# Performance work log

Measured on AMD Instinct MI355X. Metric: run time of the kernel, lower is better.

## Reference

```python
import jax, jax.numpy as jnp
import numpy as np


def _conv1x1(x, w, b):
    # x: (B, C, H, W), w: (O, C), b: (O,) -> (B, O, H, W)
    return jnp.einsum('bchw,oc->bohw', x, w) + b[None, :, None, None]


def setup_inputs() -> dict:
    key = jax.random.key(0)
    ks = jax.random.split(key, 9)
    C, Cb = 256, 128
    B, H, W = 4, 64, 64
    s_in = 1.0 / np.sqrt(C)   # kaiming-uniform-ish scale for 1x1 convs
    s_bn = 1.0 / np.sqrt(Cb)
    return {
        'x': jax.random.normal(ks[0], (B, C, H, W), dtype=jnp.float32),
        'theta_w': jax.random.uniform(ks[1], (Cb, C), jnp.float32, -s_in, s_in),
        'theta_b': jax.random.uniform(ks[2], (Cb,), jnp.float32, -s_in, s_in),
        'phi_w': jax.random.uniform(ks[3], (Cb, C), jnp.float32, -s_in, s_in),
        'phi_b': jax.random.uniform(ks[4], (Cb,), jnp.float32, -s_in, s_in),
        'g_w': jax.random.uniform(ks[5], (Cb, C), jnp.float32, -s_in, s_in),
        'g_b': jax.random.uniform(ks[6], (Cb,), jnp.float32, -s_in, s_in),
        'W_w': jax.random.uniform(ks[7], (C, Cb), jnp.float32, -s_bn, s_bn),
        'W_b': jax.random.uniform(ks[8], (C,), jnp.float32, -s_bn, s_bn),
    }


def reference(x, theta_w, theta_b, phi_w, phi_b, g_w, g_b, W_w, W_b):
    B, C, H, Wd = x.shape
    Cb = theta_w.shape[0]
    # NOTE: the original uses raw torch.reshape (row-major), NOT transpose,
    # so (B, Cb, H, W) -> (B, H*W, Cb) scrambles channel/spatial layout.
    # We replicate that exactly with jnp.reshape.
    theta = _conv1x1(x, theta_w, theta_b).reshape(B, -1, Cb)   # (B, N, Cb)
    phi = _conv1x1(x, phi_w, phi_b).reshape(B, Cb, -1)         # (B, Cb, N)
    g = _conv1x1(x, g_w, g_b).reshape(B, -1, Cb)               # (B, N, Cb)
    scores = jnp.einsum('bnc,bcm->bnm', theta, phi)            # (B, N, N)
    attn = jax.nn.softmax(scores, axis=1)                      # softmax over dim=1 (unusual axis)
    y = jnp.einsum('bnm,bmc->bnc', attn, g)                    # (B, N, Cb)
    y = y.reshape(B, -1, H, Wd)                                # raw reshape back to (B, Cb, H, W)
    w = _conv1x1(y, W_w, W_b)                                  # (B, C, H, W)
    return w + x
```

## Files before the change

kernel.cpp:

```cpp
#include <hip/hip_runtime.h>
#include <math.h>

constexpr int CI = 256;
constexpr int CB = 128;
constexpr int HWD = 4096;
constexpr int NBATCH = 4;
constexpr int NN_ = 4096;
constexpr size_t U1 = (size_t)NBATCH * NN_ * CB;
constexpr size_t U_THETA = 0;
constexpr size_t U_PHIT  = U1;
constexpr size_t U_G     = 2 * U1;
constexpr size_t U_GT    = 3 * U1;
constexpr size_t U_Y     = 4 * U1;
constexpr size_t U_XT    = 4 * U1;
constexpr size_t U_WCAT  = 8 * U1;
constexpr size_t U_WW    = 8 * U1 + 98304;
constexpr size_t F_D     = (8 * U1 + 131072) / 2;

typedef short v8s __attribute__((ext_vector_type(8)));
typedef unsigned short u8s __attribute__((ext_vector_type(8)));
typedef float v4f __attribute__((ext_vector_type(4)));
typedef float v16f __attribute__((ext_vector_type(16)));
#define MFMA16(a, b, c) __builtin_amdgcn_mfma_f32_16x16x32_bf16(a, b, c, 0, 0, 0)
#define MFMA32(a, b, c) __builtin_amdgcn_mfma_f32_32x32x16_bf16(a, b, c, 0, 0, 0)

__device__ __forceinline__ unsigned short f2bf(float f) {
    union { float f; unsigned u; } v; v.f = f;
    unsigned r = v.u + 0x7fff + ((v.u >> 16) & 1);
    return (unsigned short)(r >> 16);
}
__device__ __forceinline__ float bf2f(unsigned short s) {
    union { unsigned u; float f; } v; v.u = (unsigned)s << 16;
    return v.f;
}

__global__ __launch_bounds__(256) void k0_xpose(
    const float* __restrict__ x, unsigned short* __restrict__ xT,
    const float* __restrict__ tw, const float* __restrict__ pw,
    const float* __restrict__ gw, const float* __restrict__ Ww,
    unsigned short* __restrict__ wcat, unsigned short* __restrict__ wwB)
{
    __shared__ unsigned short T[64 * 72];
    const int t = threadIdx.x;
    if (blockIdx.y == 4) {
        int wb = blockIdx.x + 64 * blockIdx.z;
        if (t < 128) {
            int e = (wb * 128 + t) * 4;
            const float* src; unsigned short* dst;
            if (e < 32768)       { src = tw + e;           dst = wcat + e; }
            else if (e < 65536)  { src = pw + (e - 32768); dst = wcat + e; }
            else if (e < 98304)  { src = gw + (e - 65536); dst = wcat + e; }
            else                 { src = Ww + (e - 98304); dst = wwB + (e - 98304); }
            float4 f = *(const float4*)src;
            ushort4 u;
            u.x = f2bf(f.x); u.y = f2bf(f.y); u.z = f2bf(f.z); u.w = f2bf(f.w);
            *(ushort4*)dst = u;
        }
        return;
    }
    const int hw0 = blockIdx.x * 64, c0 = blockIdx.y * 64, b = blockIdx.z;
    const float* xb = x + (size_t)b * CI * HWD;
    const int rr = t >> 4, cc = t & 15;
    #pragma unroll
    for (int pass = 0; pass < 4; pass++) {
        float4 f = *(const float4*)&xb[(size_t)(c0 + pass * 16 + rr) * HWD + hw0 + cc * 4];
        T[(cc * 4 + 0) * 72 + pass * 16 + rr] = f2bf(f.x);
        T[(cc * 4 + 1) * 72 + pass * 16 + rr] = f2bf(f.y);
        T[(cc * 4 + 2) * 72 + pass * 16 + rr] = f2bf(f.z);
        T[(cc * 4 + 3) * 72 + pass * 16 + rr] = f2bf(f.w);
    }
    __syncthreads();
    const int row = t >> 2, cs = (t & 3) * 16;
    unsigned short* dst = xT + (size_t)b * NN_ * CI;
    #pragma unroll
    for (int h = 0; h < 2; h++)
        *(u8s*)&dst[(size_t)(hw0 + row) * CI + c0 + cs + h * 8] =
            *(const u8s*)&T[row * 72 + cs + h * 8];
}

__global__ __launch_bounds__(256, 4) void k1_mfma(
    const unsigned short* __restrict__ xT, const unsigned short* __restrict__ wcat,
    const float* __restrict__ tb, const float* __restrict__ pb,
    const float* __restrict__ gb,
    unsigned short* __restrict__ thetaB, unsigned short* __restrict__ phiTB,
    unsigned short* __restrict__ gB)
{
    __shared__ unsigned short LdsX[64 * 268];
    unsigned short* T = LdsX;
    const int t = threadIdx.x;
    const int lane = t & 63, w = t >> 6;
    const int l31 = lane & 31, lh = lane >> 5;
    const int qj = w >> 1, qh = w & 1;
    const int hw0 = blockIdx.x * 64, j0 = blockIdx.y * 64, b = blockIdx.z;
    const int matId = j0 >> 7, jl0 = j0 & 127;
    const float* bvec = (matId == 0) ? tb : (matId == 1) ? pb : gb;
    const unsigned short* xb = xT + (size_t)b * NN_ * CI;

    {
        const int row = t >> 2, seg = t & 3;
        #pragma unroll
        for (int c8 = 0; c8 < 8; c8++)
            *(u8s*)&LdsX[row * 268 + seg * 64 + c8 * 8] =
                *(const u8s*)&xb[(size_t)(hw0 + row) * CI + seg * 64 + c8 * 8];
    }
    __syncthreads();

    v16f s = {};
    #pragma unroll
    for (int kt = 0; kt < 16; kt++) {
        v8s a = *(const v8s*)&wcat[(size_t)(j0 + qj * 32 + l31) * CI + kt * 16 + lh * 8];
        v8s bx = *(const v8s*)&LdsX[(qh * 32 + l31) * 268 + kt * 16 + lh * 8];
        s = MFMA32(a, bx, s);
    }

    if (matId != 1) {
        unsigned short* dst = ((matId == 0) ? thetaB : gB) + (size_t)b * CB * HWD;
        #pragma unroll
        for (int reg = 0; reg < 16; reg++) {
            int row = (reg & 3) + 8 * (reg >> 2) + 4 * lh;
            int cb = jl0 + qj * 32 + row;
            dst[(size_t)cb * HWD + hw0 + qh * 32 + l31] = f2bf(s[reg] + bvec[cb]);
        }
    } else {
        __syncthreads();
        #pragma unroll
        for (int reg = 0; reg < 16; reg++) {
            int row = (reg & 3) + 8 * (reg >> 2) + 4 * lh;
            T[(qh * 32 + l31) * 76 + qj * 32 + row] =
                f2bf(s[reg] + bvec[jl0 + qj * 32 + row]);
        }
        __syncthreads();
        unsigned short* dst = phiTB + (size_t)b * NN_ * CB;
        const int row = t >> 2, cs = (t & 3) * 16;
        #pragma unroll
        for (int h = 0; h < 2; h++)
            *(u8s*)&dst[(size_t)(hw0 + row) * CB + jl0 + cs + h * 8] =
                *(const u8s*)&T[row * 76 + cs + h * 8];
    }
}

__global__ __launch_bounds__(256, 2) void k2_colsum(
    const unsigned short* __restrict__ thetaB,
    const unsigned short* __restrict__ phiTB,
    float* __restrict__ Dout)
{
    __shared__ float part[4][128];
    const int t = threadIdx.x;
    const int lane = t & 63, w = t >> 6;
    const int ln = lane & 15, quad = lane >> 4;
    const int m0 = blockIdx.x * 128, q = blockIdx.y, b = blockIdx.z;
    const unsigned short* th = thetaB + (size_t)b * NN_ * CB;
    const unsigned short* ph = phiTB + (size_t)b * NN_ * CB;

    v8s bf[8][4];
    #pragma unroll
    for (int mt = 0; mt < 8; mt++)
        #pragma unroll
        for (int kt = 0; kt < 4; kt++)
            bf[mt][kt] = *(const v8s*)&ph[(size_t)(m0 + mt * 16 + ln) * CB + kt * 32 + quad * 8];

    float dsum[8] = {};
    const int nBeg = q * 1024 + w * 16, nEnd = q * 1024 + 1024;
    v8s af[4], afn[4];
    #pragma unroll
    for (int kt = 0; kt < 4; kt++)
        af[kt] = *(const v8s*)&th[(size_t)(nBeg + ln) * CB + kt * 32 + quad * 8];
    for (int n0 = nBeg; n0 < nEnd; n0 += 64) {
        int nn = (n0 + 64 < nEnd) ? n0 + 64 : nBeg;
        #pragma unroll
        for (int kt = 0; kt < 4; kt++)
            afn[kt] = *(const v8s*)&th[(size_t)(nn + ln) * CB + kt * 32 + quad * 8];
        #pragma unroll
        for (int mt = 0; mt < 8; mt++) {
            v4f s = {};
            #pragma unroll
            for (int kt = 0; kt < 4; kt++)
                s = MFMA16(af[kt], bf[mt][kt], s);
            #pragma unroll
            for (int r = 0; r < 4; r++)
                dsum[mt] += __expf(s[r]);
        }
        #pragma unroll
        for (int kt = 0; kt < 4; kt++) af[kt] = afn[kt];
    }
    #pragma unroll
    for (int mt = 0; mt < 8; mt++) {
        float v = dsum[mt];
        v += __shfl_xor(v, 16);
        v += __shfl_xor(v, 32);
        dsum[mt] = v;
    }
    if (quad == 0) {
        #pragma unroll
        for (int mt = 0; mt < 8; mt++) part[w][mt * 16 + ln] = dsum[mt];
    }
    __syncthreads();
    if (t < 128) {
        float v = part[0][t] + part[1][t] + part[2][t] + part[3][t];
        Dout[((size_t)q * NBATCH + b) * NN_ + m0 + t] = v;
    }
}

__global__ __launch_bounds__(256) void k1b_transpose_scale_g(
    const unsigned short* __restrict__ gB, const float* __restrict__ D,
    unsigned short* __restrict__ gTB)
{
    __shared__ unsigned short T[128 * 36];
    const int t = threadIdx.x;
    const int m0 = blockIdx.x * 32;
    const int b  = blockIdx.z;
    const unsigned short* F = gB + (size_t)b * CB * HWD;
    unsigned short* dst = gTB + (size_t)b * CB * HWD;
    const int mrow = t >> 3, cg = t & 7;
    {
        int m = m0 + mrow;
        float d = D[((size_t)0 * NBATCH + b) * NN_ + m]
                + D[((size_t)1 * NBATCH + b) * NN_ + m]
                + D[((size_t)2 * NBATCH + b) * NN_ + m]
                + D[((size_t)3 * NBATCH + b) * NN_ + m];
        float r = 1.0f / d;
        #pragma unroll
        for (int j8 = 0; j8 < 2; j8++) {
            int cbase = cg * 8 + j8 * 64;
            u8s u = *(const u8s*)&F[(size_t)m * CB + cbase];
            #pragma unroll
            for (int e = 0; e < 8; e++)
                T[(cbase + e) * 36 + mrow] = f2bf(bf2f(u[e]) * r);
        }
    }
    __syncthreads();
    const int c = t >> 1, mh = (t & 1) * 16;
    #pragma unroll
    for (int h8 = 0; h8 < 2; h8++)
        *(u8s*)&dst[(size_t)c * HWD + m0 + mh + h8 * 8] =
            *(const u8s*)&T[c * 36 + mh + h8 * 8];
}

__global__ __launch_bounds__(256, 3) void k3_attn(
    const unsigned short* __restrict__ thetaB,
    const unsigned short* __restrict__ phiTB,
    const unsigned short* __restrict__ gTB,
    unsigned short* __restrict__ Y)
{
    __shared__ unsigned short Lphi[2][64 * 132];
    __shared__ unsigned short Pl[2][64 * 68];
    const int t = threadIdx.x;
    const int lane = t & 63, w = t >> 6;
    const int l31 = lane & 31, lh = lane >> 5;
    const int qn = w & 1, qm = w >> 1;
    const int rowS = t >> 4, colS = t & 15;
    const int n0 = blockIdx.x * 64, q = blockIdx.y, b = blockIdx.z;
    const unsigned short* th = thetaB + (size_t)b * NN_ * CB;
    const unsigned short* ph = phiTB + (size_t)b * NN_ * CB;
    const unsigned short* gT = gTB + (size_t)b * CB * HWD;

    v8s ath[8];
    #pragma unroll
    for (int kt = 0; kt < 8; kt++)
        ath[kt] = *(const v8s*)&th[(size_t)(n0 + qn * 32 + l31) * CB + kt * 16 + lh * 8];

    const int mBeg = q * 1024;
    v8s preg[4];
    #pragma unroll
    for (int pass = 0; pass < 4; pass++)
        preg[pass] = *(const v8s*)&ph[(size_t)(mBeg + pass * 16 + rowS) * CB + colS * 8];
    #pragma unroll
    for (int pass = 0; pass < 4; pass++)
        *(v8s*)&Lphi[0][(pass * 16 + rowS) * 132 + colS * 8] = preg[pass];
    #pragma unroll
    for (int pass = 0; pass < 4; pass++)
        preg[pass] = *(const v8s*)&ph[(size_t)(mBeg + 64 + pass * 16 + rowS) * CB + colS * 8];
    __syncthreads();

    v16f yacc[2] = {};
    #pragma unroll 2
    for (int it = 0; it < 16; ++it) {
        const int cur = it & 1;
        const int m0 = mBeg + it * 64;
        v8s gfrag[4];
        #pragma unroll
        for (int ks = 0; ks < 4; ks++)
            gfrag[ks] = *(const v8s*)&gT[(size_t)(w * 32 + l31) * HWD + m0 + ks * 16 + lh * 8];
        v16f s = {};
        #pragma unroll
        for (int kt = 0; kt < 8; kt++) {
            v8s bphi = *(const v8s*)&Lphi[cur][(qm * 32 + l31) * 132 + kt * 16 + lh * 8];
            s = MFMA32(ath[kt], bphi, s);
        }
        #pragma unroll
        for (int pass = 0; pass < 4; pass++)
            *(v8s*)&Lphi[cur ^ 1][(pass * 16 + rowS) * 132 + colS * 8] = preg[pass];
        #pragma unroll
        for (int reg = 0; reg < 16; reg++) {
            int row = qn * 32 + (reg & 3) + 8 * (reg >> 2) + 4 * lh;
            Pl[cur][row * 68 + qm * 32 + l31] = f2bf(__expf(s[reg]));
        }
        __syncthreads();
        const int mP = mBeg + ((it + 2) & 15) * 64;
        #pragma unroll
        for (int pass = 0; pass < 4; pass++)
            preg[pass] = *(const v8s*)&ph[(size_t)(mP + pass * 16 + rowS) * CB + colS * 8];
        #pragma unroll
        for (int ks = 0; ks < 4; ks++)
            #pragma unroll
            for (int nt = 0; nt < 2; nt++) {
                v8s ap = *(const v8s*)&Pl[cur][(nt * 32 + l31) * 68 + ks * 16 + lh * 8];
                yacc[nt] = MFMA32(ap, gfrag[ks], yacc[nt]);
            }
    }
    unsigned short* yp = Y + ((size_t)q * NBATCH + b) * CB * HWD;
    #pragma unroll
    for (int nt = 0; nt < 2; nt++)
        #pragma unroll
        for (int reg = 0; reg < 16; reg++) {
            int row = (reg & 3) + 8 * (reg >> 2) + 4 * lh;
            yp[(size_t)(n0 + nt * 32 + row) * CB + w * 32 + l31] = f2bf(yacc[nt][reg]);
        }
}

__global__ __launch_bounds__(256, 2) void k4_mfma(
    const float* __restrict__ x, const unsigned short* __restrict__ wwB,
    const float* __restrict__ Wb, const unsigned short* __restrict__ Ybuf,
    float* __restrict__ out)
{
    __shared__ unsigned short Yt[64 * 136];
    const int t = threadIdx.x;
    const int lane = t & 63, w = t >> 6;
    const int ln = lane & 15, quad = lane >> 4;
    const int hw0 = blockIdx.x * 64, o0 = blockIdx.y * 128, b = blockIdx.z;

    const int cb = t >> 1, seg = (t & 1) * 32;
    #pragma unroll
    for (int g8 = 0; g8 < 4; g8++) {
        float sum[8] = {};
        #pragma unroll
        for (int q = 0; q < 4; q++) {
            u8s u = *(const u8s*)&Ybuf[((size_t)q * NBATCH + b) * CB * HWD +
                                       (size_t)cb * HWD + hw0 + seg + g8 * 8];
            #pragma unroll
            for (int j = 0; j < 8; j++) sum[j] += bf2f(u[j]);
        }
        #pragma unroll
        for (int j = 0; j < 8; j++)
            Yt[(seg + g8 * 8 + j) * 136 + cb] = f2bf(sum[j]);
    }
    __syncthreads();

    v8s aw[2][4];
    #pragma unroll
    for (int os = 0; os < 2; os++)
        #pragma unroll
        for (int kt = 0; kt < 4; kt++)
            aw[os][kt] = *(const v8s*)&wwB[(size_t)(o0 + w * 32 + os * 16 + ln) * CB + kt * 32 + quad * 8];

    v4f s[2][4] = {};
    #pragma unroll
    for (int kt = 0; kt < 4; kt++) {
        v8s by[4];
        #pragma unroll
        for (int mt = 0; mt < 4; mt++)
            by[mt] = *(const v8s*)&Yt[(mt * 16 + ln) * 136 + kt * 32 + quad * 8];
        #pragma unroll
        for (int os = 0; os < 2; os++)
            #pragma unroll
            for (int mt = 0; mt < 4; mt++)
                s[os][mt] = MFMA16(aw[os][kt], by[mt], s[os][mt]);
    }
    #pragma unroll
    for (int os = 0; os < 2; os++)
        #pragma unroll
        for (int mt = 0; mt < 4; mt++)
            #pragma unroll
            for (int r = 0; r < 4; r++) {
                int o = o0 + w * 32 + os * 16 + quad * 4 + r;
                size_t idx = (size_t)b * CI * HWD + (size_t)o * HWD + hw0 + mt * 16 + ln;
                out[idx] = s[os][mt][r] + Wb[o] + x[idx];
            }
}

extern "C" void kernel_launch(void* const* d_in, const int* in_sizes, int n_in,
                              void* d_out, int out_size, void* d_ws, size_t ws_size,
                              hipStream_t stream)
{
    const float* x  = (const float*)d_in[0];
    const float* tw = (const float*)d_in[1];
    const float* tb = (const float*)d_in[2];
    const float* pw = (const float*)d_in[3];
    const float* pb = (const float*)d_in[4];
    const float* gw = (const float*)d_in[5];
    const float* gb = (const float*)d_in[6];
    const float* Ww = (const float*)d_in[7];
    const float* Wb = (const float*)d_in[8];
    unsigned short* wsu = (unsigned short*)d_ws;
    float* wsf = (float*)d_ws;
    unsigned short* thetaB = wsu + U_THETA;
    unsigned short* phiTB  = wsu + U_PHIT;
    unsigned short* gB     = wsu + U_G;
    unsigned short* gTB    = wsu + U_GT;
    unsigned short* Ybuf   = wsu + U_Y;
    unsigned short* xTB    = wsu + U_XT;
    unsigned short* wcatB  = wsu + U_WCAT;
    unsigned short* wwB    = wsu + U_WW;
    float* Dbuf = wsf + F_D;
    float* out = (float*)d_out;
    dim3 blk(256, 1, 1);
    hipLaunchKernelGGL(k0_xpose, dim3(64, 5, NBATCH), blk, 0, stream,
                       x, xTB, tw, pw, gw, Ww, wcatB, wwB);
    hipLaunchKernelGGL(k1_mfma, dim3(64, 6, NBATCH), blk, 0, stream,
                       xTB, wcatB, tb, pb, gb, thetaB, phiTB, gB);
    hipLaunchKernelGGL(k2_colsum, dim3(32, 4, NBATCH), blk, 0, stream,
                       thetaB, phiTB, Dbuf);
    hipLaunchKernelGGL(k1b_transpose_scale_g, dim3(128, 1, NBATCH), blk, 0, stream,
                       gB, Dbuf, gTB);
    hipLaunchKernelGGL(k3_attn, dim3(64, 4, NBATCH), blk, 0, stream,
                       thetaB, phiTB, gTB, Ybuf);
    hipLaunchKernelGGL(k4_mfma, dim3(64, 2, NBATCH), blk, 0, stream,
                       x, wwB, Wb, Ybuf, out);
}
```

Measured before the change: 196.3 us.

## Keep attention probabilities in registers via permlane32 swap, widen n-tile to 128

```diff
diff --git a/kernel.cpp b/kernel.cpp
--- a/kernel.cpp
+++ b/kernel.cpp
@@ -19,6 +19,7 @@
 
 typedef short v8s __attribute__((ext_vector_type(8)));
 typedef unsigned short u8s __attribute__((ext_vector_type(8)));
+typedef unsigned int v4u __attribute__((ext_vector_type(4)));
 typedef float v4f __attribute__((ext_vector_type(4)));
 typedef float v16f __attribute__((ext_vector_type(16)));
 #define MFMA16(a, b, c) __builtin_amdgcn_mfma_f32_16x16x32_bf16(a, b, c, 0, 0, 0)
@@ -32,6 +33,22 @@
 __device__ __forceinline__ float bf2f(unsigned short s) {
     union { unsigned u; float f; } v; v.u = (unsigned)s << 16;
     return v.f;
+}
+__device__ __forceinline__ unsigned pack2bf(float lo, float hi) {
+    return (unsigned)f2bf(lo) | ((unsigned)f2bf(hi) << 16);
+}
+__device__ __forceinline__ void pl32swap(unsigned &a, unsigned &b) {
+    asm volatile("v_permlane32_swap_b32 %0, %1" : "+v"(a), "+v"(b));
+}
+__device__ __forceinline__ v8s pack_swap(float p0, float p1, float p2, float p3,
+                                         float p4, float p5, float p6, float p7) {
+    unsigned c0 = pack2bf(p0, p1), c1 = pack2bf(p2, p3);
+    unsigned c2 = pack2bf(p4, p5), c3 = pack2bf(p6, p7);
+    pl32swap(c0, c2);
+    pl32swap(c1, c3);
+    union { v4u u; v8s s; } r;
+    r.u[0] = c0; r.u[1] = c1; r.u[2] = c2; r.u[3] = c3;
+    return r.s;
 }
 
 __global__ __launch_bounds__(256) void k0_xpose(
@@ -236,20 +253,18 @@
             *(const u8s*)&T[c * 36 + mh + h8 * 8];
 }
 
-__global__ __launch_bounds__(256, 3) void k3_attn(
+__global__ __launch_bounds__(256, 2) void k3_attn(
     const unsigned short* __restrict__ thetaB,
     const unsigned short* __restrict__ phiTB,
     const unsigned short* __restrict__ gTB,
     unsigned short* __restrict__ Y)
 {
-    __shared__ unsigned short Lphi[2][64 * 132];
-    __shared__ unsigned short Pl[2][64 * 68];
+    __shared__ unsigned short Lphi[2][64 * 134];
     const int t = threadIdx.x;
     const int lane = t & 63, w = t >> 6;
     const int l31 = lane & 31, lh = lane >> 5;
-    const int qn = w & 1, qm = w >> 1;
     const int rowS = t >> 4, colS = t & 15;
-    const int n0 = blockIdx.x * 64, q = blockIdx.y, b = blockIdx.z;
+    const int n0 = blockIdx.x * 128, q = blockIdx.y, b = blockIdx.z;
     const unsigned short* th = thetaB + (size_t)b * NN_ * CB;
     const unsigned short* ph = phiTB + (size_t)b * NN_ * CB;
     const unsigned short* gT = gTB + (size_t)b * CB * HWD;
@@ -257,64 +272,80 @@
     v8s ath[8];
     #pragma unroll
     for (int kt = 0; kt < 8; kt++)
-        ath[kt] = *(const v8s*)&th[(size_t)(n0 + qn * 32 + l31) * CB + kt * 16 + lh * 8];
+        ath[kt] = *(const v8s*)&th[(size_t)(n0 + w * 32 + l31) * CB + kt * 16 + lh * 8];
 
     const int mBeg = q * 1024;
     v8s preg[4];
     #pragma unroll
-    for (int pass = 0; pass < 4; pass++)
-        preg[pass] = *(const v8s*)&ph[(size_t)(mBeg + pass * 16 + rowS) * CB + colS * 8];
-    #pragma unroll
-    for (int pass = 0; pass < 4; pass++)
-        *(v8s*)&Lphi[0][(pass * 16 + rowS) * 132 + colS * 8] = preg[pass];
-    #pragma unroll
-    for (int pass = 0; pass < 4; pass++)
-        preg[pass] = *(const v8s*)&ph[(size_t)(mBeg + 64 + pass * 16 + rowS) * CB + colS * 8];
-    __syncthreads();
-
-    v16f yacc[2] = {};
+    for (int p = 0; p < 4; p++)
+        preg[p] = *(const v8s*)&ph[(size_t)(mBeg + p * 16 + rowS) * CB + colS * 8];
+    #pragma unroll
+    for (int p = 0; p < 4; p++)
+        *(v8s*)&Lphi[0][(p * 16 + rowS) * 134 + colS * 8] = preg[p];
+    #pragma unroll
+    for (int p = 0; p < 4; p++)
+        preg[p] = *(const v8s*)&ph[(size_t)(mBeg + 64 + p * 16 + rowS) * CB + colS * 8];
+    __syncthreads();
+
+    v16f yacc[4] = {};
     #pragma unroll 2
     for (int it = 0; it < 16; ++it) {
         const int cur = it & 1;
         const int m0 = mBeg + it * 64;
-        v8s gfrag[4];
-        #pragma unroll
-        for (int ks = 0; ks < 4; ks++)
-            gfrag[ks] = *(const v8s*)&gT[(size_t)(w * 32 + l31) * HWD + m0 + ks * 16 + lh * 8];
-        v16f s = {};
+        v8s gfA[2][4];
+        #pragma unroll
+        for (int ks = 0; ks < 2; ks++)
+            #pragma unroll
+            for (int ct = 0; ct < 4; ct++)
+                gfA[ks][ct] = *(const v8s*)&gT[(size_t)(ct * 32 + l31) * HWD + m0 + ks * 16 + lh * 8];
+        v16f st0 = {}, st1 = {};
         #pragma unroll
         for (int kt = 0; kt < 8; kt++) {
-            v8s bphi = *(const v8s*)&Lphi[cur][(qm * 32 + l31) * 132 + kt * 16 + lh * 8];
-            s = MFMA32(ath[kt], bphi, s);
-        }
-        #pragma unroll
-        for (int pass = 0; pass < 4; pass++)
-            *(v8s*)&Lphi[cur ^ 1][(pass * 16 + rowS) * 132 + colS * 8] = preg[pass];
-        #pragma unroll
-        for (int reg = 0; reg < 16; reg++) {
-            int row = qn * 32 + (reg & 3) + 8 * (reg >> 2) + 4 * lh;
-            Pl[cur][row * 68 + qm * 32 + l31] = f2bf(__expf(s[reg]));
-        }
+            v8s a0 = *(const v8s*)&Lphi[cur][(l31) * 134 + kt * 16 + lh * 8];
+            v8s a1 = *(const v8s*)&Lphi[cur][(32 + l31) * 134 + kt * 16 + lh * 8];
+            st0 = MFMA32(a0, ath[kt], st0);
+            st1 = MFMA32(a1, ath[kt], st1);
+        }
+        #pragma unroll
+        for (int p = 0; p < 4; p++)
+            *(v8s*)&Lphi[cur ^ 1][(p * 16 + rowS) * 134 + colS * 8] = preg[p];
         __syncthreads();
-        const int mP = mBeg + ((it + 2) & 15) * 64;
-        #pragma unroll
-        for (int pass = 0; pass < 4; pass++)
-            preg[pass] = *(const v8s*)&ph[(size_t)(mP + pass * 16 + rowS) * CB + colS * 8];
-        #pragma unroll
-        for (int ks = 0; ks < 4; ks++)
-            #pragma unroll
-            for (int nt = 0; nt < 2; nt++) {
-                v8s ap = *(const v8s*)&Pl[cur][(nt * 32 + l31) * 68 + ks * 16 + lh * 8];
-                yacc[nt] = MFMA32(ap, gfrag[ks], yacc[nt]);
-            }
+        {
+            const int mP = mBeg + ((it + 2) & 15) * 64;
+            #pragma unroll
+            for (int p = 0; p < 4; p++)
+                preg[p] = *(const v8s*)&ph[(size_t)(mP + p * 16 + rowS) * CB + colS * 8];
+        }
+        v8s gfB[2][4];
+        #pragma unroll
+        for (int ks = 0; ks < 2; ks++)
+            #pragma unroll
+            for (int ct = 0; ct < 4; ct++)
+                gfB[ks][ct] = *(const v8s*)&gT[(size_t)(ct * 32 + l31) * HWD + m0 + 32 + ks * 16 + lh * 8];
+        v8s apv0 = pack_swap(__expf(st0[0]),  __expf(st0[1]),  __expf(st0[2]),  __expf(st0[3]),
+                             __expf(st0[4]),  __expf(st0[5]),  __expf(st0[6]),  __expf(st0[7]));
+        v8s apv1 = pack_swap(__expf(st0[8]),  __expf(st0[9]),  __expf(st0[10]), __expf(st0[11]),
+                             __expf(st0[12]), __expf(st0[13]), __expf(st0[14]), __expf(st0[15]));
+        v8s apv2 = pack_swap(__expf(st1[0]),  __expf(st1[1]),  __expf(st1[2]),  __expf(st1[3]),
+                             __expf(st1[4]),  __expf(st1[5]),  __expf(st1[6]),  __expf(st1[7]));
+        v8s apv3 = pack_swap(__expf(st1[8]),  __expf(st1[9]),  __expf(st1[10]), __expf(st1[11]),
+                             __expf(st1[12]), __expf(st1[13]), __expf(st1[14]), __expf(st1[15]));
+        #pragma unroll
+        for (int ct = 0; ct < 4; ct++) yacc[ct] = MFMA32(apv0, gfA[0][ct], yacc[ct]);
+        #pragma unroll
+        for (int ct = 0; ct < 4; ct++) yacc[ct] = MFMA32(apv1, gfA[1][ct], yacc[ct]);
+        #pragma unroll
+        for (int ct = 0; ct < 4; ct++) yacc[ct] = MFMA32(apv2, gfB[0][ct], yacc[ct]);
+        #pragma unroll
+        for (int ct = 0; ct < 4; ct++) yacc[ct] = MFMA32(apv3, gfB[1][ct], yacc[ct]);
     }
     unsigned short* yp = Y + ((size_t)q * NBATCH + b) * CB * HWD;
     #pragma unroll
-    for (int nt = 0; nt < 2; nt++)
+    for (int ct = 0; ct < 4; ct++)
         #pragma unroll
         for (int reg = 0; reg < 16; reg++) {
             int row = (reg & 3) + 8 * (reg >> 2) + 4 * lh;
-            yp[(size_t)(n0 + nt * 32 + row) * CB + w * 32 + l31] = f2bf(yacc[nt][reg]);
+            yp[(size_t)(n0 + w * 32 + row) * CB + ct * 32 + l31] = f2bf(yacc[ct][reg]);
         }
 }
 
@@ -412,7 +443,7 @@
                        thetaB, phiTB, Dbuf);
     hipLaunchKernelGGL(k1b_transpose_scale_g, dim3(128, 1, NBATCH), blk, 0, stream,
                        gB, Dbuf, gTB);
-    hipLaunchKernelGGL(k3_attn, dim3(64, 4, NBATCH), blk, 0, stream,
+    hipLaunchKernelGGL(k3_attn, dim3(32, 4, NBATCH), blk, 0, stream,
                        thetaB, phiTB, gTB, Ybuf);
     hipLaunchKernelGGL(k4_mfma, dim3(64, 2, NBATCH), blk, 0, stream,
                        x, wwB, Wb, Ybuf, out);
```

Result: slower. 211.4 us (+7.7%).
